# Optimization experiments

Hardware: AMD Instinct MI355X
Metric: run time of the kernel (lower is better)

Reference implementation:

```python
import math
import jax, jax.numpy as jnp
import numpy as np

D = 1024
H = 16
DK = D // H
B = 4
L = 2048


def setup_inputs() -> dict:
    key = jax.random.key(0)
    ks = jax.random.split(key, 11)
    s = 1.0 / math.sqrt(D)
    return {
        "q": jax.random.normal(ks[0], (B, L, D), jnp.float32),
        "k": jax.random.normal(ks[1], (B, L, D), jnp.float32),
        "v": jax.random.normal(ks[2], (B, L, D), jnp.float32),
        "wq_w": jax.random.normal(ks[3], (D, D), jnp.float32) * s,
        "wq_b": jnp.zeros((D,), jnp.float32),
        "wk_w": jax.random.normal(ks[4], (D, D), jnp.float32) * s,
        "wk_b": jnp.zeros((D,), jnp.float32),
        "wv_w": jax.random.normal(ks[5], (D, D), jnp.float32) * s,
        "wv_b": jnp.zeros((D,), jnp.float32),
        "wo_w": jax.random.normal(ks[6], (D, D), jnp.float32) * s,
        "wo_b": jnp.zeros((D,), jnp.float32),
    }


def reference(q, k, v, wq_w, wq_b, wk_w, wk_b, wv_w, wv_b, wo_w, wo_b):
    # torch Linear: x @ W.T + b
    Q = (q @ wq_w.T + wq_b).reshape(B, L, H, DK).transpose(0, 2, 1, 3)  # [B,H,L,DK]
    K = (k @ wk_w.T + wk_b).reshape(B, -1, H, DK).transpose(0, 2, 1, 3)
    V = (v @ wv_w.T + wv_b).reshape(B, -1, H, DK).transpose(0, 2, 1, 3)
    sc = jnp.einsum("bhqd,bhkd->bhqk", Q, K) / math.sqrt(DK)  # [B,H,L,L]
    # causal mask: strictly upper triangular filled with -1e9
    cm = jnp.triu(jnp.ones((L, L), dtype=bool), 1)
    sc = jnp.where(cm, jnp.float32(-1e9), sc)
    at = jax.nn.softmax(sc, axis=-1)  # dropout p=0 (eval)
    out = jnp.einsum("bhqk,bhkd->bhqd", at, V)  # [B,H,L,DK]
    out = out.transpose(0, 2, 1, 3).reshape(B, L, D)
    return out @ wo_w.T + wo_b
```

## Files before the change

kernel.cpp:

```cpp
#include <hip/hip_runtime.h>
#include <stdint.h>

#define DD 1024
#define NH 16
#define DHEAD 64
#define NB 4
#define SEQ 2048
#define MR (NB*SEQ)
#define NT (SEQ/128)
#define NKT (DD/64)

typedef __attribute__((ext_vector_type(8))) short s8v;
typedef __attribute__((ext_vector_type(4))) float f4v;

__device__ __forceinline__ unsigned short f2bf(float f) {
  union { float f; uint32_t u; } c; c.f = f;
  uint32_t u = c.u;
  u += 0x7fffu + ((u >> 16) & 1u);
  return (unsigned short)(u >> 16);
}
__device__ __forceinline__ unsigned short f2bf_trunc(float f) {
  union { float f; uint32_t u; } c; c.f = f;
  return (unsigned short)(c.u >> 16);
}

__device__ __forceinline__ void load_lds16(const void* g, void* lds) {
  __builtin_amdgcn_global_load_lds(
      (__attribute__((address_space(1))) void*)(uintptr_t)g,
      (__attribute__((address_space(3))) void*)(uint32_t)(uintptr_t)lds,
      16, 0, 0);
}

__global__ void cvt_all(
    const float* __restrict__ w0, const float* __restrict__ w1,
    const float* __restrict__ w2, const float* __restrict__ w3,
    const float* __restrict__ a0, const float* __restrict__ a1,
    const float* __restrict__ a2,
    unsigned short* __restrict__ dw0, unsigned short* __restrict__ dw1,
    unsigned short* __restrict__ dw2, unsigned short* __restrict__ dw3,
    unsigned short* __restrict__ da0, unsigned short* __restrict__ da1,
    unsigned short* __restrict__ da2)
{
  int blk = blockIdx.x;
  const float* src;
  unsigned short* dst;
  size_t i;
  if (blk < 2048) {
    int a = blk >> 9;
    src = a == 0 ? w0 : (a == 1 ? w1 : (a == 2 ? w2 : w3));
    dst = a == 0 ? dw0 : (a == 1 ? dw1 : (a == 2 ? dw2 : dw3));
    i = (size_t)(blk & 511) * 2048 + (size_t)threadIdx.x * 8;
  } else {
    int blk2 = blk - 2048;
    int a = blk2 >> 12;
    src = a == 0 ? a0 : (a == 1 ? a1 : a2);
    dst = a == 0 ? da0 : (a == 1 ? da1 : da2);
    i = (size_t)(blk2 & 4095) * 2048 + (size_t)threadIdx.x * 8;
  }
  float4 a4 = *(const float4*)(src + i);
  float4 b4 = *(const float4*)(src + i + 4);
  union { unsigned short us[8]; uint4 u; } t;
  t.us[0] = f2bf(a4.x); t.us[1] = f2bf(a4.y); t.us[2] = f2bf(a4.z); t.us[3] = f2bf(a4.w);
  t.us[4] = f2bf(b4.x); t.us[5] = f2bf(b4.y); t.us[6] = f2bf(b4.z); t.us[7] = f2bf(b4.w);
  *(uint4*)(dst + i) = t.u;
}

#define STAGE_AB(kt, bufi)                                                     \
  for (int i_ = 0; i_ < 4; i_++) {                                             \
    int c_ = tid + i_ * 256; int row_ = c_ >> 3, pg_ = c_ & 7;                 \
    load_lds16(Ab + (size_t)row_ * DD + (kt) * 64 + ((pg_ ^ (row_ & 7)) << 3), \
               &As[bufi][c_ * 8]);                                             \
  }                                                                            \
  for (int i_ = 0; i_ < 4; i_++) {                                             \
    int c_ = tid + i_ * 256; int row_ = c_ >> 3, pg_ = c_ & 7;                 \
    load_lds16(Bb + (size_t)row_ * DD + (kt) * 64 + ((pg_ ^ (row_ & 7)) << 3), \
               &Bs[bufi][c_ * 8]);                                             \
  }

#define GEMM_KLOOP                                                             \
  STAGE_AB(0, 0);                                                              \
  STAGE_AB(1, 1);                                                              \
  for (int t = 0; t < NKT; t++) {                                              \
    if (t < NKT - 1) asm volatile("s_waitcnt vmcnt(8)" ::: "memory");          \
    else             asm volatile("s_waitcnt vmcnt(0)" ::: "memory");          \
    __builtin_amdgcn_sched_barrier(0);                                         \
    __builtin_amdgcn_s_barrier();                                              \
    __builtin_amdgcn_sched_barrier(0);                                         \
    const short* Al = As[t & 1];                                               \
    const short* Bl = Bs[t & 1];                                               \
    for (int kk = 0; kk < 64; kk += 32) {                                      \
      int gb = kk >> 3;                                                        \
      s8v af[4], bf[4];                                                        \
      for (int i = 0; i < 4; i++)                                              \
        af[i] = *(const s8v*)(Al + (wm + i * 16 + lr) * 64 + (((gb + lg) ^ sw) << 3)); \
      for (int i = 0; i < 4; i++)                                              \
        bf[i] = *(const s8v*)(Bl + (wn + i * 16 + lr) * 64 + (((gb + lg) ^ sw) << 3)); \
      for (int mi = 0; mi < 4; mi++)                                           \
        for (int ni = 0; ni < 4; ni++)                                         \
          acc[mi][ni] = __builtin_amdgcn_mfma_f32_16x16x32_bf16(af[mi], bf[ni], acc[mi][ni], 0, 0, 0); \
    }                                                                          \
    __builtin_amdgcn_sched_barrier(0);                                         \
    __builtin_amdgcn_s_barrier();                                              \
    __builtin_amdgcn_sched_barrier(0);                                         \
    if (t + 2 < NKT) { STAGE_AB(t + 2, t & 1); }                               \
  }

__global__ __launch_bounds__(256, 2) void gemm_bt(
    const unsigned short* __restrict__ A,
    const unsigned short* __restrict__ Bw,
    const float* __restrict__ bias,
    float* __restrict__ Cout)
{
  __shared__ __align__(16) short As[2][128 * 64];
  __shared__ __align__(16) short Bs[2][128 * 64];
  const int linear = blockIdx.y * 8 + blockIdx.x;
  const int nx = linear >> 6;
  const int my = linear & 63;
  const int tid = threadIdx.x;
  const int wave = tid >> 6, lane = tid & 63;
  const int wm = (wave >> 1) * 64, wn = (wave & 1) * 64;
  const int lr = lane & 15, lg = lane >> 4;
  const int sw = lr & 7;
  const unsigned short* Ab = A + (size_t)my * 128 * DD;
  const unsigned short* Bb = Bw + (size_t)nx * 128 * DD;

  f4v z = {0.f, 0.f, 0.f, 0.f};
  f4v acc[4][4];
  for (int mi = 0; mi < 4; mi++) for (int ni = 0; ni < 4; ni++) acc[mi][ni] = z;

  GEMM_KLOOP

  for (int ni = 0; ni < 4; ni++) {
    int col = nx * 128 + wn + ni * 16 + lr;
    float bv = bias[col];
    for (int mi = 0; mi < 4; mi++) {
      int row0 = my * 128 + wm + mi * 16 + lg * 4;
      for (int r = 0; r < 4; r++)
        Cout[(size_t)(row0 + r) * DD + col] = acc[mi][ni][r] + bv;
    }
  }
}

__global__ __launch_bounds__(256, 2) void gemm_qkv(
    const unsigned short* __restrict__ qA, const unsigned short* __restrict__ kA,
    const unsigned short* __restrict__ vA,
    const unsigned short* __restrict__ wq, const unsigned short* __restrict__ wk,
    const unsigned short* __restrict__ wv,
    const float* __restrict__ bq, const float* __restrict__ bk, const float* __restrict__ bv,
    unsigned short* __restrict__ Qp, unsigned short* __restrict__ Kp,
    unsigned short* __restrict__ VpT)
{
  __shared__ __align__(16) short As[2][128 * 64];
  __shared__ __align__(16) short Bs[2][128 * 64];
  const int linear = blockIdx.y * 24 + blockIdx.x;
  const int nx  = linear / 192;
  const int rem = linear % 192;
  const int seg = rem >> 6;
  const int my  = rem & 63;
  const unsigned short* A  = seg == 0 ? qA : (seg == 1 ? kA : vA);
  const unsigned short* Bw = seg == 0 ? wq : (seg == 1 ? wk : wv);
  const float* bias        = seg == 0 ? bq : (seg == 1 ? bk : bv);

  const int tid = threadIdx.x;
  const int wave = tid >> 6, lane = tid & 63;
  const int wm = (wave >> 1) * 64, wn = (wave & 1) * 64;
  const int lr = lane & 15, lg = lane >> 4;
  const int sw = lr & 7;
  const unsigned short* Ab = A + (size_t)my * 128 * DD;
  const unsigned short* Bb = Bw + (size_t)nx * 128 * DD;

  f4v z = {0.f, 0.f, 0.f, 0.f};
  f4v acc[4][4];
  for (int mi = 0; mi < 4; mi++) for (int ni = 0; ni < 4; ni++) acc[mi][ni] = z;

  GEMM_KLOOP

  if (seg < 2) {
    unsigned short* Cout = seg == 0 ? Qp : Kp;
    for (int ni = 0; ni < 4; ni++) {
      int col = nx * 128 + wn + ni * 16 + lr;
      float bv = bias[col];
      for (int mi = 0; mi < 4; mi++) {
        int row0 = my * 128 + wm + mi * 16 + lg * 4;
        for (int r = 0; r < 4; r++)
          Cout[(size_t)(row0 + r) * DD + col] = f2bf(acc[mi][ni][r] + bv);
      }
    }
  } else {
    for (int ni = 0; ni < 4; ni++) {
      int col = nx * 128 + wn + ni * 16 + lr;
      float bv = bias[col];
      int hh = col >> 6, dd = col & 63;
      for (int mi = 0; mi < 4; mi++) {
        int row0 = my * 128 + wm + mi * 16 + lg * 4;
        int bb = row0 >> 11, ll = row0 & 2047;
        uint64_t w = 0;
        for (int r = 0; r < 4; r++)
          w |= (uint64_t)f2bf(acc[mi][ni][r] + bv) << (16 * r);
        *(uint64_t*)(VpT + ((size_t)(bb * NH + hh) * 64 + dd) * SEQ + ll) = w;
      }
    }
  }
}

#define KS_STRIDE 72
#define VT_STRIDE 136
#define PS_STRIDE 72

__device__ __forceinline__ void attn_step(
    const s8v (&qf)[2][2], const s8v (&kf)[2][4],
    f4v (&o)[2][4], float (&ls)[2][4],
    int qbase, int colbase,
    const short* __restrict__ Vt, int vsub, short* __restrict__ Pw,
    int lr, int lg)
{
  const float csc = 0.125f * 1.44269504089f;
  const float FM = 14.0f;
  f4v zv = {0.f, 0.f, 0.f, 0.f};
  f4v s[2][4];
  for (int mi = 0; mi < 2; mi++) for (int ni = 0; ni < 4; ni++) s[mi][ni] = zv;
  __builtin_amdgcn_s_setprio(1);
  for (int ks = 0; ks < 2; ks++)
    for (int mi = 0; mi < 2; mi++)
      for (int ni = 0; ni < 4; ni++)
        s[mi][ni] = __builtin_amdgcn_mfma_f32_16x16x32_bf16(qf[mi][ks], kf[ks][ni], s[mi][ni], 0, 0, 0);
  __builtin_amdgcn_s_setprio(0);
  const bool diag = (colbase + 63 > qbase);
  for (int mi = 0; mi < 2; mi++)
    for (int ni = 0; ni < 4; ni++)
      for (int r = 0; r < 4; r++) {
        float e = __builtin_amdgcn_exp2f(fmaf(s[mi][ni][r], csc, -FM));
        if (diag) {
          int row = qbase + mi * 16 + lg * 4 + r;
          int col = colbase + ni * 16 + lr;
          e = (col > row) ? 0.f : e;
        }
        ls[mi][r] += e;
        Pw[(mi * 16 + lg * 4 + r) * PS_STRIDE + ni * 16 + lr] = (short)f2bf_trunc(e);
      }
  for (int kc2 = 0; kc2 < 2; kc2++) {
    s8v pf[2], vf[4];
    for (int mi = 0; mi < 2; mi++)
      pf[mi] = *(const s8v*)(Pw + (mi * 16 + lr) * PS_STRIDE + kc2 * 32 + lg * 8);
    for (int ni = 0; ni < 4; ni++)
      vf[ni] = *(const s8v*)(Vt + (ni * 16 + lr) * VT_STRIDE + vsub + kc2 * 32 + lg * 8);
    __builtin_amdgcn_s_setprio(1);
    for (int mi = 0; mi < 2; mi++)
      for (int ni = 0; ni < 4; ni++)
        o[mi][ni] = __builtin_amdgcn_mfma_f32_16x16x32_bf16(pf[mi], vf[ni], o[mi][ni], 0, 0, 0);
    __builtin_amdgcn_s_setprio(0);
  }
}

__global__ __launch_bounds__(256, 2) void fattn(
    const unsigned short* __restrict__ Qp,
    const unsigned short* __restrict__ Kp,
    const unsigned short* __restrict__ VpT,
    unsigned short* __restrict__ Op)
{
  __shared__ __align__(16) short Ks[128 * KS_STRIDE];
  __shared__ __align__(16) short Vt[64 * VT_STRIDE];
  __shared__ __align__(16) short Ps[4 * 32 * PS_STRIDE];
  const int tid = threadIdx.x;
  const int wave = tid >> 6, lane = tid & 63;
  const int lr = lane & 15, lg = lane >> 4;
  const int linear = blockIdx.y * 8 + blockIdx.x;
  const int xA = linear >> 6;
  const int bh = linear & 63;
  const int b = bh >> 4, h = bh & 15;
  const int xB = NT - 1 - xA;
  const int qbA = xA * 128 + wave * 32;
  const int qbB = xB * 128 + wave * 32;
  const unsigned short* Qrow = Qp + ((size_t)b * SEQ) * DD + h * DHEAD;
  const unsigned short* Krow = Kp + ((size_t)b * SEQ) * DD + h * DHEAD;
  const unsigned short* VT   = VpT + (size_t)bh * 64 * SEQ;
  short* Pw = Ps + wave * (32 * PS_STRIDE);

  s8v qfA[2][2], qfB[2][2];
  for (int mi = 0; mi < 2; mi++)
    for (int ks = 0; ks < 2; ks++) {
      qfA[mi][ks] = *(const s8v*)(Qrow + (size_t)(qbA + mi * 16 + lr) * DD + ks * 32 + lg * 8);
      qfB[mi][ks] = *(const s8v*)(Qrow + (size_t)(qbB + mi * 16 + lr) * DD + ks * 32 + lg * 8);
    }

  f4v zv = {0.f, 0.f, 0.f, 0.f};
  f4v oA[2][4], oB[2][4];
  float lA[2][4], lB[2][4];
  for (int mi = 0; mi < 2; mi++)
    for (int r = 0; r < 4; r++) { lA[mi][r] = 0.f; lB[mi][r] = 0.f; }
  for (int mi = 0; mi < 2; mi++)
    for (int ni = 0; ni < 4; ni++) { oA[mi][ni] = zv; oB[mi][ni] = zv; }

  const int npair = xB + 1;

  for (int p = 0; p < npair; p++) {
    s8v kreg[4], vreg[4];
    int krow[4], kkc[4], vd[4], vkc[4];
    for (int i = 0; i < 4; i++) {
      int c = tid + i * 256;
      krow[i] = c >> 3; kkc[i] = (c & 7) << 3;
      kreg[i] = *(const s8v*)(Krow + (size_t)(p * 128 + krow[i]) * DD + kkc[i]);
      vd[i] = c >> 4; vkc[i] = (c & 15) << 3;
      vreg[i] = *(const s8v*)(VT + (size_t)vd[i] * SEQ + p * 128 + vkc[i]);
    }
    __syncthreads();
    for (int i = 0; i < 4; i++) {
      *(s8v*)(Ks + krow[i] * KS_STRIDE + kkc[i]) = kreg[i];
      *(s8v*)(Vt + vd[i] * VT_STRIDE + vkc[i]) = vreg[i];
    }
    __syncthreads();
    for (int sub = 0; sub < 2; sub++) {
      int colbase = (2 * p + sub) * 64;
      bool actB = colbase <= qbB + 31;
      bool actA = colbase <= qbA + 31;
      if (actB || actA) {
        const short* KsSub = Ks + sub * 64 * KS_STRIDE;
        s8v kf[2][4];
        for (int ks = 0; ks < 2; ks++)
          for (int ni = 0; ni < 4; ni++)
            kf[ks][ni] = *(const s8v*)(KsSub + (ni * 16 + lr) * KS_STRIDE + ks * 32 + lg * 8);
        int vsub = sub * 64;
        if (actB) attn_step(qfB, kf, oB, lB, qbB, colbase, Vt, vsub, Pw, lr, lg);
        if (actA) attn_step(qfA, kf, oA, lA, qbA, colbase, Vt, vsub, Pw, lr, lg);
      }
    }
  }

  unsigned short* Orow = Op + ((size_t)b * SEQ) * DD + h * DHEAD;
  for (int mi = 0; mi < 2; mi++)
    for (int r = 0; r < 4; r++) {
      float sA = lA[mi][r], sB = lB[mi][r];
      for (int d2 = 1; d2 < 16; d2 <<= 1) {
        sA += __shfl_xor(sA, d2);
        sB += __shfl_xor(sB, d2);
      }
      float invA = 1.f / sA, invB = 1.f / sB;
      size_t rowA = (size_t)qbA + mi * 16 + lg * 4 + r;
      size_t rowB = (size_t)qbB + mi * 16 + lg * 4 + r;
      for (int ni = 0; ni < 4; ni++) {
        Orow[rowA * DD + ni * 16 + lr] = f2bf(oA[mi][ni][r] * invA);
        Orow[rowB * DD + ni * 16 + lr] = f2bf(oB[mi][ni][r] * invB);
      }
    }
}

extern "C" void kernel_launch(void* const* d_in, const int* in_sizes, int n_in,
                              void* d_out, int out_size, void* d_ws, size_t ws_size,
                              hipStream_t stream) {
  const float* q    = (const float*)d_in[0];
  const float* k    = (const float*)d_in[1];
  const float* v    = (const float*)d_in[2];
  const float* wq_w = (const float*)d_in[3];
  const float* wq_b = (const float*)d_in[4];
  const float* wk_w = (const float*)d_in[5];
  const float* wk_b = (const float*)d_in[6];
  const float* wv_w = (const float*)d_in[7];
  const float* wv_b = (const float*)d_in[8];
  const float* wo_w = (const float*)d_in[9];
  const float* wo_b = (const float*)d_in[10];

  const size_t BIG = (size_t)MR * DD;
  const size_t WSZ = (size_t)DD * DD;
  unsigned short* p = (unsigned short*)d_ws;
  unsigned short* wqb = p; p += WSZ;
  unsigned short* wkb = p; p += WSZ;
  unsigned short* wvb = p; p += WSZ;
  unsigned short* wob = p; p += WSZ;
  unsigned short* Qp  = p; p += BIG;
  unsigned short* Kp  = p; p += BIG;
  unsigned short* VpT = p; p += BIG;
  unsigned short* AO  = p; p += BIG;

  unsigned short* qb = AO;
  unsigned short* kb = (unsigned short*)d_out;
  unsigned short* vb = kb + BIG;

  cvt_all<<<dim3(14336), dim3(256), 0, stream>>>(
      wq_w, wk_w, wv_w, wo_w, q, k, v,
      wqb, wkb, wvb, wob, qb, kb, vb);

  gemm_qkv<<<dim3(24, MR / 128), dim3(256), 0, stream>>>(
      qb, kb, vb, wqb, wkb, wvb, wq_b, wk_b, wv_b, Qp, Kp, VpT);

  fattn<<<dim3(NT / 2, NB * NH), dim3(256), 0, stream>>>(Qp, Kp, VpT, AO);

  gemm_bt<<<dim3(8, MR / 128), dim3(256), 0, stream>>>(AO, wob, wo_b, (float*)d_out);

  (void)in_sizes; (void)n_in; (void)out_size; (void)ws_size;
}
```

Baseline: 302.8 us.

## Double-buffer K/V tiles with direct global-to-LDS loads and XOR swizzle

Replaces the register-staged K/V tile loads with asynchronous global-to-LDS copies (load_lds16) into two LDS buffers, prefetching two tiles ahead and using vmcnt waits plus barriers to pipeline loads with compute. Padded LDS strides are replaced by XOR-swizzled layouts for K, V and the P scratch to avoid bank conflicts without padding. This is meant to hide global memory latency behind the MFMA work. In exchange it doubles K/V LDS use, which may affect occupancy, and relies on exact vmcnt counting for correctness.

```diff
diff --git a/kernel.cpp b/kernel.cpp
--- a/kernel.cpp
+++ b/kernel.cpp
@@ -203,16 +203,12 @@
   }
 }
 
-#define KS_STRIDE 72
-#define VT_STRIDE 136
-#define PS_STRIDE 72
-
 __device__ __forceinline__ void attn_step(
     const s8v (&qf)[2][2], const s8v (&kf)[2][4],
     f4v (&o)[2][4], float (&ls)[2][4],
     int qbase, int colbase,
-    const short* __restrict__ Vt, int vsub, short* __restrict__ Pw,
-    int lr, int lg)
+    const short* __restrict__ Vb, int sub, short* __restrict__ Pw,
+    int lr, int lg, int sw)
 {
   const float csc = 0.125f * 1.44269504089f;
   const float FM = 14.0f;
@@ -236,14 +232,16 @@
           e = (col > row) ? 0.f : e;
         }
         ls[mi][r] += e;
-        Pw[(mi * 16 + lg * 4 + r) * PS_STRIDE + ni * 16 + lr] = (short)f2bf_trunc(e);
+        Pw[(mi * 16 + lg * 4 + r) * 64 +
+           ((((ni << 1) + (lr >> 3)) ^ ((lg * 4 + r) & 7)) << 3) + (lr & 7)] =
+            (short)f2bf_trunc(e);
       }
   for (int kc2 = 0; kc2 < 2; kc2++) {
     s8v pf[2], vf[4];
     for (int mi = 0; mi < 2; mi++)
-      pf[mi] = *(const s8v*)(Pw + (mi * 16 + lr) * PS_STRIDE + kc2 * 32 + lg * 8);
+      pf[mi] = *(const s8v*)(Pw + (mi * 16 + lr) * 64 + (((kc2 * 4 + lg) ^ sw) << 3));
     for (int ni = 0; ni < 4; ni++)
-      vf[ni] = *(const s8v*)(Vt + (ni * 16 + lr) * VT_STRIDE + vsub + kc2 * 32 + lg * 8);
+      vf[ni] = *(const s8v*)(Vb + (ni * 16 + lr) * 128 + (((sub * 8 + kc2 * 4 + lg) ^ sw) << 3));
     __builtin_amdgcn_s_setprio(1);
     for (int mi = 0; mi < 2; mi++)
       for (int ni = 0; ni < 4; ni++)
@@ -252,18 +250,31 @@
   }
 }
 
+#define STAGE_KV(pp, bufi)                                                     \
+  for (int i_ = 0; i_ < 4; i_++) {                                             \
+    int c_ = tid + i_ * 256; int kr_ = c_ >> 3, kg_ = c_ & 7;                  \
+    load_lds16(Krow + (size_t)((pp) * 128 + kr_) * DD + ((kg_ ^ (kr_ & 7)) << 3), \
+               &Ks[bufi][c_ * 8]);                                             \
+  }                                                                            \
+  for (int i_ = 0; i_ < 4; i_++) {                                             \
+    int c_ = tid + i_ * 256; int vr_ = c_ >> 4, vg_ = c_ & 15;                 \
+    load_lds16(VT + (size_t)vr_ * SEQ + (pp) * 128 + ((vg_ ^ (vr_ & 7)) << 3), \
+               &Vt[bufi][c_ * 8]);                                             \
+  }
+
 __global__ __launch_bounds__(256, 2) void fattn(
     const unsigned short* __restrict__ Qp,
     const unsigned short* __restrict__ Kp,
     const unsigned short* __restrict__ VpT,
     unsigned short* __restrict__ Op)
 {
-  __shared__ __align__(16) short Ks[128 * KS_STRIDE];
-  __shared__ __align__(16) short Vt[64 * VT_STRIDE];
-  __shared__ __align__(16) short Ps[4 * 32 * PS_STRIDE];
+  __shared__ __align__(16) short Ks[2][128 * 64];
+  __shared__ __align__(16) short Vt[2][64 * 128];
+  __shared__ __align__(16) short Ps[4 * 32 * 64];
   const int tid = threadIdx.x;
   const int wave = tid >> 6, lane = tid & 63;
   const int lr = lane & 15, lg = lane >> 4;
+  const int sw = lr & 7;
   const int linear = blockIdx.y * 8 + blockIdx.x;
   const int xA = linear >> 6;
   const int bh = linear & 63;
@@ -274,7 +285,7 @@
   const unsigned short* Qrow = Qp + ((size_t)b * SEQ) * DD + h * DHEAD;
   const unsigned short* Krow = Kp + ((size_t)b * SEQ) * DD + h * DHEAD;
   const unsigned short* VT   = VpT + (size_t)bh * 64 * SEQ;
-  short* Pw = Ps + wave * (32 * PS_STRIDE);
+  short* Pw = Ps + wave * (32 * 64);
 
   s8v qfA[2][2], qfB[2][2];
   for (int mi = 0; mi < 2; mi++)
@@ -293,37 +304,35 @@
 
   const int npair = xB + 1;
 
+  STAGE_KV(0, 0);
+  STAGE_KV(1, 1);
+
   for (int p = 0; p < npair; p++) {
-    s8v kreg[4], vreg[4];
-    int krow[4], kkc[4], vd[4], vkc[4];
-    for (int i = 0; i < 4; i++) {
-      int c = tid + i * 256;
-      krow[i] = c >> 3; kkc[i] = (c & 7) << 3;
-      kreg[i] = *(const s8v*)(Krow + (size_t)(p * 128 + krow[i]) * DD + kkc[i]);
-      vd[i] = c >> 4; vkc[i] = (c & 15) << 3;
-      vreg[i] = *(const s8v*)(VT + (size_t)vd[i] * SEQ + p * 128 + vkc[i]);
-    }
-    __syncthreads();
-    for (int i = 0; i < 4; i++) {
-      *(s8v*)(Ks + krow[i] * KS_STRIDE + kkc[i]) = kreg[i];
-      *(s8v*)(Vt + vd[i] * VT_STRIDE + vkc[i]) = vreg[i];
-    }
-    __syncthreads();
+    if (p < npair - 1) asm volatile("s_waitcnt vmcnt(8)" ::: "memory");
+    else               asm volatile("s_waitcnt vmcnt(0)" ::: "memory");
+    __builtin_amdgcn_sched_barrier(0);
+    __builtin_amdgcn_s_barrier();
+    __builtin_amdgcn_sched_barrier(0);
+    const short* Kb = Ks[p & 1];
+    const short* Vb = Vt[p & 1];
     for (int sub = 0; sub < 2; sub++) {
       int colbase = (2 * p + sub) * 64;
       bool actB = colbase <= qbB + 31;
       bool actA = colbase <= qbA + 31;
       if (actB || actA) {
-        const short* KsSub = Ks + sub * 64 * KS_STRIDE;
+        const short* KsSub = Kb + sub * 64 * 64;
         s8v kf[2][4];
         for (int ks = 0; ks < 2; ks++)
           for (int ni = 0; ni < 4; ni++)
-            kf[ks][ni] = *(const s8v*)(KsSub + (ni * 16 + lr) * KS_STRIDE + ks * 32 + lg * 8);
-        int vsub = sub * 64;
-        if (actB) attn_step(qfB, kf, oB, lB, qbB, colbase, Vt, vsub, Pw, lr, lg);
-        if (actA) attn_step(qfA, kf, oA, lA, qbA, colbase, Vt, vsub, Pw, lr, lg);
-      }
-    }
+            kf[ks][ni] = *(const s8v*)(KsSub + (ni * 16 + lr) * 64 + (((ks * 4 + lg) ^ sw) << 3));
+        if (actB) attn_step(qfB, kf, oB, lB, qbB, colbase, Vb, sub, Pw, lr, lg, sw);
+        if (actA) attn_step(qfA, kf, oA, lA, qbA, colbase, Vb, sub, Pw, lr, lg, sw);
+      }
+    }
+    __builtin_amdgcn_sched_barrier(0);
+    __builtin_amdgcn_s_barrier();
+    __builtin_amdgcn_sched_barrier(0);
+    if (p + 2 < npair) { STAGE_KV(p + 2, p & 1); }
   }
 
   unsigned short* Orow = Op + ((size_t)b * SEQ) * DD + h * DHEAD;
```

Result: no change. 306.1 us (+1.1%).
